# Kernel optimization log

Hardware: AMD Instinct MI355X
Metric: run time of the kernel (lower is better)

Reference implementation:

```python
import jax, jax.numpy as jnp
import numpy as np

N_NODES = 50000
N_EDGES = 800000
HIDDEN = 128
N_TYPES = 4
TIME_STEPS = [2]  # one layer, 2 propagation steps; residuals = {}


def setup_inputs() -> dict:
    key = jax.random.key(0)
    ks = jax.random.split(key, 8)
    std = HIDDEN ** (-0.5)
    states = jax.random.normal(ks[0], (N_NODES, HIDDEN), dtype=jnp.float32)
    etype = jax.random.randint(ks[1], (N_EDGES,), 0, N_TYPES, dtype=jnp.int32)
    src = jax.random.randint(ks[2], (N_EDGES,), 0, N_NODES, dtype=jnp.int32)
    tgt = jax.random.randint(ks[3], (N_EDGES,), 0, N_NODES, dtype=jnp.int32)
    edges = jnp.stack([etype, src, tgt], axis=1)  # [E, 3]: (type, source, target)
    type_weights = std * jax.random.normal(ks[4], (N_TYPES, HIDDEN, HIDDEN), dtype=jnp.float32)
    type_biases = std * jax.random.normal(ks[5], (N_TYPES, HIDDEN), dtype=jnp.float32)
    # Keras GRUCell (reset_after=True): kernel [H,3H], recurrent_kernel [H,3H], bias [2,3H]
    gru_kernel = std * jax.random.normal(ks[6], (HIDDEN, 3 * HIDDEN), dtype=jnp.float32)
    k7, k8 = jax.random.split(ks[7])
    gru_rec_kernel = std * jax.random.normal(k7, (HIDDEN, 3 * HIDDEN), dtype=jnp.float32)
    gru_bias = std * jax.random.normal(k8, (2, 3 * HIDDEN), dtype=jnp.float32)
    return {"states": states, "edges": edges, "type_weights": type_weights,
            "type_biases": type_biases, "gru_kernel": gru_kernel,
            "gru_rec_kernel": gru_rec_kernel, "gru_bias": gru_bias}


def _gru_cell(x, h, kernel, rec_kernel, bias):
    # Keras GRUCell with reset_after=True, tanh / sigmoid activations
    mx = x @ kernel + bias[0]          # [N, 3H]
    mh = h @ rec_kernel + bias[1]      # [N, 3H]
    xz, xr, xh = jnp.split(mx, 3, axis=-1)
    rz, rr, rh = jnp.split(mh, 3, axis=-1)
    z = jax.nn.sigmoid(xz + rz)
    r = jax.nn.sigmoid(xr + rr)
    hh = jnp.tanh(xh + r * rh)
    return z * h + (1.0 - z) * hh


def _propagate(h, etype, src, tgt, type_weights, type_biases, kernel, rec_kernel, bias):
    n_nodes = h.shape[0]
    xs = h[src]  # [E, H] gather of source states
    msg_e = jnp.zeros_like(xs)
    for t in range(N_TYPES):  # small fixed loop over edge types
        mask = (etype == t).astype(h.dtype)[:, None]
        msg_e = msg_e + mask * (xs @ type_weights[t] + type_biases[t])
    messages = jax.ops.segment_sum(msg_e, tgt, num_segments=n_nodes)  # scatter-add
    return _gru_cell(messages, h, kernel, rec_kernel, bias)


def reference(states, edges, type_weights, type_biases, gru_kernel, gru_rec_kernel, gru_bias):
    etype, src, tgt = edges[:, 0], edges[:, 1], edges[:, 2]
    h = states
    for steps in TIME_STEPS:  # single layer here (residuals empty)
        for _ in range(steps):
            h = _propagate(h, etype, src, tgt, type_weights, type_biases,
                           gru_kernel, gru_rec_kernel, gru_bias)
    return h
```

## Files before the change

### kernel.cpp

```cpp
#include <hip/hip_runtime.h>
#include <stdint.h>

namespace {
constexpr int kNodes = 50000;
constexpr int kEdges = 800000;
constexpr int kHid   = 128;
constexpr int kScanBlocks = (kNodes + 255) / 256;
constexpr int kBlocks64 = (kNodes + 63) / 64;

constexpr size_t oCounts    = 0;
constexpr size_t oCursor    = 200704;
constexpr size_t oBlockSums = 401408;
constexpr size_t oBpack     = 402432;
constexpr size_t oPacked    = 1057792;
constexpr size_t oMsg      = 4257792;
constexpr size_t oAux       = 17057792;
constexpr size_t oY         = 29857792;
constexpr size_t kWsNeeded   = oY + 51200000;
constexpr size_t kWsFallback = oY;

constexpr size_t bKhi = 0,      bKlo = 98304,  bRhi = 196608,
                 bRlo = 294912, bWhi = 393216, bWlo = 524288;
}

typedef __attribute__((ext_vector_type(8))) short short8;
typedef __attribute__((ext_vector_type(4))) float f32x4;

union ABFrag { short8 v; uint16_t u[8]; uint4 q; };

__device__ __forceinline__ uint16_t f2bf(float x) {
  uint32_t u = __float_as_uint(x);
  return (uint16_t)((u + 0x7FFFu + ((u >> 16) & 1u)) >> 16);
}
__device__ __forceinline__ float bf2f(uint16_t h) {
  return __uint_as_float(((uint32_t)h) << 16);
}

__device__ __forceinline__ float fast_rcp(float x) {
#if __has_builtin(__builtin_amdgcn_rcpf)
  return __builtin_amdgcn_rcpf(x);
#else
  return 1.f / x;
#endif
}
__device__ __forceinline__ float fast_exp2(float x) {
#if __has_builtin(__builtin_amdgcn_exp2f)
  return __builtin_amdgcn_exp2f(x);
#else
  return exp2f(x);
#endif
}
__device__ __forceinline__ float sigf(float x) {
  return fast_rcp(1.f + fast_exp2(-1.4426950408889634f * x));
}
__device__ __forceinline__ float tanh_fast(float x) {
  x = fminf(fmaxf(x, -10.f), 10.f);
  const float t = fast_exp2(2.8853900817779268f * x);
  return (t - 1.f) * fast_rcp(t + 1.f);
}

__device__ __forceinline__ int swz_pi(int p) {
  return (p & 64) | ((p & 3) << 4) | ((p >> 2) & 15);
}


__global__ __launch_bounds__(256) void count_kernel(const int* __restrict__ edges,
                                                    int* __restrict__ counts) {
  int e = blockIdx.x * 256 + threadIdx.x;
  if (e < kEdges) atomicAdd(&counts[edges[e * 3 + 2]], 1);
}

__global__ __launch_bounds__(256) void scan1_kernel(const int* __restrict__ counts,
                                                    int* __restrict__ cursor,
                                                    int* __restrict__ blocksums) {
  __shared__ int sd[256];
  const int t = threadIdx.x;
  const int i = blockIdx.x * 256 + t;
  int v = (i < kNodes) ? counts[i] : 0;
  sd[t] = v;
  __syncthreads();
  for (int off = 1; off < 256; off <<= 1) {
    int x = (t >= off) ? sd[t - off] : 0;
    __syncthreads();
    sd[t] += x;
    __syncthreads();
  }
  if (i < kNodes) cursor[i] = sd[t] - v;
  if (t == 255) blocksums[blockIdx.x] = sd[255];
}

__global__ __launch_bounds__(256) void scan2_kernel(int* __restrict__ blocksums,
                                                    int* __restrict__ boff,
                                                    int* __restrict__ bcur) {
  __shared__ int sd[256];
  const int t = threadIdx.x;
  int v = (t < kScanBlocks) ? blocksums[t] : 0;
  sd[t] = v;
  __syncthreads();
  for (int off = 1; off < 256; off <<= 1) {
    int x = (t >= off) ? sd[t - off] : 0;
    __syncthreads();
    sd[t] += x;
    __syncthreads();
  }
  if (t < kScanBlocks) {
    const int excl = sd[t] - v;
    blocksums[t] = excl;
    boff[t] = excl;
    bcur[t] = excl;
  }
  if (t == 0) boff[kScanBlocks] = kEdges;
}

__global__ __launch_bounds__(256) void scan3_kernel(int* __restrict__ cursor,
                                                    const int* __restrict__ blocksums) {
  const int i = blockIdx.x * 256 + threadIdx.x;
  if (i < kNodes) cursor[i] += blocksums[blockIdx.x];
}

__global__ __launch_bounds__(256) void bucket_scatter(
    const int* __restrict__ edges,
    int* __restrict__ bcur,
    unsigned long long* __restrict__ bkt) {
  __shared__ int hist[kScanBlocks];
  __shared__ int base[kScanBlocks];
  const int tid = threadIdx.x;
  const int e0 = blockIdx.x * 16000;
  const int e1 = min(e0 + 16000, kEdges);
  if (tid < kScanBlocks) hist[tid] = 0;
  __syncthreads();
  for (int e = e0 + tid; e < e1; e += 256)
    atomicAdd(&hist[edges[e * 3 + 2] >> 8], 1);
  __syncthreads();
  if (tid < kScanBlocks) {
    base[tid] = atomicAdd(&bcur[tid], hist[tid]);
    hist[tid] = 0;
  }
  __syncthreads();
  for (int e = e0 + tid; e < e1; e += 256) {
    const int et  = edges[e * 3 + 0];
    const int src = edges[e * 3 + 1];
    const int tgt = edges[e * 3 + 2];
    const int b = tgt >> 8;
    const int idx = atomicAdd(&hist[b], 1);
    bkt[base[b] + idx] =
        ((unsigned long long)(unsigned)tgt << 32) | (unsigned)(src * 4 + et);
  }
}

__global__ __launch_bounds__(256) void bucket_fill(
    const unsigned long long* __restrict__ bkt,
    const int* __restrict__ boff,
    const int* __restrict__ rowstart,
    unsigned* __restrict__ packed) {
  __shared__ int lcur[256];
  const int tid = threadIdx.x;
  const int b = blockIdx.x;
  const int nbase = b * 256;
  lcur[tid] = (nbase + tid < kNodes) ? rowstart[nbase + tid] : 0;
  __syncthreads();
  const int lo = boff[b], hi = boff[b + 1];
  for (int i = lo + tid; i < hi; i += 256) {
    const unsigned long long ent = bkt[i];
    const int tgt = (int)(ent >> 32);
    const int pos = atomicAdd(&lcur[tgt & 255], 1);
    packed[pos] = (unsigned)ent;
  }
}

__global__ __launch_bounds__(256) void fill_kernel(const int* __restrict__ edges,
                                                   int* __restrict__ cursor,
                                                   unsigned* __restrict__ packed) {
  int e = blockIdx.x * 256 + threadIdx.x;
  if (e < kEdges) {
    const int et  = edges[e * 3 + 0];
    const int src = edges[e * 3 + 1];
    const int tgt = edges[e * 3 + 2];
    const int pos = atomicAdd(&cursor[tgt], 1);
    packed[pos] = (unsigned)(src * 4 + et);
  }
}

__global__ __launch_bounds__(256) void pack_b_kernel(
    const float* __restrict__ K,
    const float* __restrict__ R,
    const float* __restrict__ W,
    uint16_t* __restrict__ bp) {
  const int idx = blockIdx.x * 256 + threadIdx.x;
  uint16_t* khi = bp + bKhi / 2;
  uint16_t* klo = bp + bKlo / 2;
  uint16_t* rhi = bp + bRhi / 2;
  uint16_t* rlo = bp + bRlo / 2;
  uint16_t* whi = bp + bWhi / 2;
  uint16_t* wlo = bp + bWlo / 2;
  if (idx < 128 * 384) {
    const int k = idx / 384, c = idx % 384;
    const int ksrc = swz_pi(k);
    const int kt = k >> 5, quad = (k >> 3) & 3, j = k & 7;
    const int nt = c >> 4, ln = (c & 15) | (quad << 4);
    const size_t o = ((size_t)(kt * 24 + nt) * 64 + ln) * 8 + j;
    const float kv = K[ksrc * 384 + c];
    const float rv = R[k * 384 + c];
    const uint16_t kh = f2bf(kv), rh = f2bf(rv);
    khi[o] = kh; klo[o] = f2bf(kv - bf2f(kh));
    rhi[o] = rh; rlo[o] = f2bf(rv - bf2f(rh));
  } else if (idx < 128 * 384 + 128 * 512) {
    const int i2 = idx - 128 * 384;
    const int k = i2 / 512, c = i2 % 512;
    const int t = c >> 7, cc = c & 127;
    const float wv = W[((size_t)t * 128 + k) * 128 + cc];
    const int kt = k >> 5, quad = (k >> 3) & 3, j = k & 7;
    const int nt = c >> 4, ln = (c & 15) | (quad << 4);
    const size_t o = ((size_t)(kt * 32 + nt) * 64 + ln) * 8 + j;
    const uint16_t wh = f2bf(wv);
    whi[o] = wh; wlo[o] = f2bf(wv - bf2f(wh));
  }
}

__device__ __forceinline__ void split8(const float* p, ABFrag& hi, ABFrag& lo) {
  const float4 a0 = *(const float4*)p;
  const float4 a1 = *(const float4*)(p + 4);
  const float v[8] = {a0.x, a0.y, a0.z, a0.w, a1.x, a1.y, a1.z, a1.w};
#pragma unroll
  for (int j = 0; j < 8; ++j) {
    const uint16_t t = f2bf(v[j]);
    hi.u[j] = t; lo.u[j] = f2bf(v[j] - bf2f(t));
  }
}
__device__ __forceinline__ void conv8(const float* p, ABFrag& hi) {
  const float4 a0 = *(const float4*)p;
  const float4 a1 = *(const float4*)(p + 4);
  const float v[8] = {a0.x, a0.y, a0.z, a0.w, a1.x, a1.y, a1.z, a1.w};
#pragma unroll
  for (int j = 0; j < 8; ++j) hi.u[j] = f2bf(v[j]);
}

__global__ __launch_bounds__(256, 3) void transform_mfma(
    const float* __restrict__ h,
    const uint16_t* __restrict__ bp,
    const float* __restrict__ TB,
    uint16_t* __restrict__ y16) {
  const int tid = threadIdx.x;
  const int w = tid >> 6;
  const int lane = tid & 63;
  const int col16 = lane & 15, quad = lane >> 4;
  const int b = blockIdx.x;
  const int half = (b >> 3) & 1;
  const int ng = (b & 7) | ((b >> 4) << 3);
  const int node0 = ng * 64;

  const uint4* __restrict__ Whi = (const uint4*)(bp + bWhi / 2);

  bool mok[4];
#pragma unroll
  for (int m = 0; m < 4; ++m) mok[m] = (node0 + m * 16) < kNodes;
  if (!mok[0]) return;

  f32x4 acc[4][4];
#pragma unroll
  for (int s = 0; s < 4; ++s)
#pragma unroll
    for (int m = 0; m < 4; ++m) acc[s][m] = (f32x4){0.f, 0.f, 0.f, 0.f};

  const float* hrow = h + (size_t)(node0 + col16) * kHid + quad * 8;

#pragma unroll
  for (int kt = 0; kt < 4; ++kt) {
    ABFrag ah[4], al[4];
#pragma unroll
    for (int m = 0; m < 4; ++m) {
      if (mok[m]) {
        split8(hrow + (size_t)m * 16 * kHid + kt * 32, ah[m], al[m]);
      } else {
        ah[m].q = make_uint4(0, 0, 0, 0); al[m].q = ah[m].q;
      }
    }
#pragma unroll
    for (int s = 0; s < 4; ++s) {
      ABFrag bh;
      bh.q = Whi[(size_t)(kt * 32 + w * 8 + half * 4 + s) * 64 + lane];
#pragma unroll
      for (int m = 0; m < 4; ++m) {
        f32x4 c = acc[s][m];
        c = __builtin_amdgcn_mfma_f32_16x16x32_bf16(ah[m].v, bh.v, c, 0, 0, 0);
        c = __builtin_amdgcn_mfma_f32_16x16x32_bf16(al[m].v, bh.v, c, 0, 0, 0);
        acc[s][m] = c;
      }
    }
  }

  float bias[4];
#pragma unroll
  for (int s = 0; s < 4; ++s) bias[s] = TB[w * 128 + (half * 4 + s) * 16 + col16];
#pragma unroll
  for (int m = 0; m < 4; ++m) {
    if (!mok[m]) continue;
#pragma unroll
    for (int r = 0; r < 4; ++r) {
      const int node = node0 + m * 16 + quad * 4 + r;
      const uint32_t lo = (uint32_t)f2bf(acc[0][m][r] + bias[0]) |
                          ((uint32_t)f2bf(acc[1][m][r] + bias[1]) << 16);
      const uint32_t hi = (uint32_t)f2bf(acc[2][m][r] + bias[2]) |
                          ((uint32_t)f2bf(acc[3][m][r] + bias[3]) << 16);
      const unsigned long long val = ((unsigned long long)hi << 32) | lo;
      __builtin_nontemporal_store(
          val, (unsigned long long*)&y16[(size_t)node * 512 + w * 128 +
                                         half * 64 + col16 * 4]);
    }
  }
}

__global__ __launch_bounds__(256) void gather_kernel(
    const uint32_t* __restrict__ y2,
    const uint32_t* __restrict__ packed,
    const int* __restrict__ rowstart,
    const int* __restrict__ counts,
    uint32_t* __restrict__ msg2) {
  const int tid = threadIdx.x;
  const int lane = tid & 63;
  const int v = blockIdx.x * 4 + (tid >> 6);
  const int cnt = counts[v];
  const int s0 = rowstart[v];
  float a0 = 0.f, a1 = 0.f;
  int e = 0;
  for (; e + 8 <= cnt; e += 8) {
    uint32_t p[8], u[8];
#pragma unroll
    for (int i = 0; i < 8; ++i) p[i] = packed[s0 + e + i];
#pragma unroll
    for (int i = 0; i < 8; ++i) u[i] = y2[(size_t)p[i] * 64 + lane];
#pragma unroll
    for (int i = 0; i < 8; ++i) {
      a0 += __uint_as_float(u[i] << 16);
      a1 += __uint_as_float(u[i] & 0xFFFF0000u);
    }
  }
  for (; e < cnt; ++e) {
    const uint32_t p = packed[s0 + e];
    const uint32_t u = y2[(size_t)p * 64 + lane];
    a0 += __uint_as_float(u << 16);
    a1 += __uint_as_float(u & 0xFFFF0000u);
  }
  msg2[(size_t)v * 64 + lane] = (uint32_t)f2bf(a0) | ((uint32_t)f2bf(a1) << 16);
}

__global__ __launch_bounds__(256, 2) void gru_mfma(
    const uint16_t* __restrict__ msg16,
    const float* __restrict__ hin,
    const uint16_t* __restrict__ bp,
    const float* __restrict__ gb,
    float* __restrict__ hout) {
  const int tid = threadIdx.x;
  const int w = tid >> 6;
  const int lane = tid & 63;
  const int col16 = lane & 15, quad = lane >> 4;
  const int node0 = blockIdx.x * 64;

  const uint4* __restrict__ Khi = (const uint4*)(bp + bKhi / 2);
  const uint4* __restrict__ Klo = (const uint4*)(bp + bKlo / 2);
  const uint4* __restrict__ Rhi = (const uint4*)(bp + bRhi / 2);
  const uint4* __restrict__ Rlo = (const uint4*)(bp + bRlo / 2);

  bool mok[4];
#pragma unroll
  for (int m = 0; m < 4; ++m) mok[m] = (node0 + m * 16) < kNodes;

  f32x4 aZ[2][4], aR[2][4], aX[2][4], aH[2][4];
#pragma unroll
  for (int i = 0; i < 2; ++i)
#pragma unroll
    for (int m = 0; m < 4; ++m) {
      aZ[i][m] = (f32x4){0.f, 0.f, 0.f, 0.f};
      aR[i][m] = aZ[i][m]; aX[i][m] = aZ[i][m]; aH[i][m] = aZ[i][m];
    }

  const uint16_t* mrow = msg16 + (size_t)(node0 + col16) * kHid + quad * 8;
  const float* hrow = hin + (size_t)(node0 + col16) * kHid + quad * 8;

#pragma unroll
  for (int kt = 0; kt < 4; ++kt) {
    ABFrag mh[4], hh[4];
#pragma unroll
    for (int m = 0; m < 4; ++m) {
      if (mok[m]) {
        mh[m].q = *(const uint4*)(mrow + (size_t)m * 16 * kHid + kt * 32);
        conv8(hrow + (size_t)m * 16 * kHid + kt * 32, hh[m]);
      } else {
        mh[m].q = make_uint4(0, 0, 0, 0); hh[m].q = mh[m].q;
      }
    }
#pragma unroll
    for (int lnt = 0; lnt < 2; ++lnt) {
      const int ntc = w * 2 + lnt;
      const size_t oz = (size_t)(kt * 24 + ntc) * 64 + lane;
      const size_t orr = (size_t)(kt * 24 + 8 + ntc) * 64 + lane;
      const size_t oh = (size_t)(kt * 24 + 16 + ntc) * 64 + lane;
      ABFrag kzh, kzl, rzh, rzl, krh, krl, rrh, rrl, khh, khl, rhh, rhl;
      kzh.q = Khi[oz]; kzl.q = Klo[oz]; rzh.q = Rhi[oz]; rzl.q = Rlo[oz];
      krh.q = Khi[orr]; krl.q = Klo[orr]; rrh.q = Rhi[orr]; rrl.q = Rlo[orr];
      khh.q = Khi[oh]; khl.q = Klo[oh]; rhh.q = Rhi[oh]; rhl.q = Rlo[oh];
#pragma unroll
      for (int m = 0; m < 4; ++m) {
        f32x4 z = aZ[lnt][m];
        z = __builtin_amdgcn_mfma_f32_16x16x32_bf16(mh[m].v, kzh.v, z, 0, 0, 0);
        z = __builtin_amdgcn_mfma_f32_16x16x32_bf16(mh[m].v, kzl.v, z, 0, 0, 0);
        z = __builtin_amdgcn_mfma_f32_16x16x32_bf16(hh[m].v, rzh.v, z, 0, 0, 0);
        z = __builtin_amdgcn_mfma_f32_16x16x32_bf16(hh[m].v, rzl.v, z, 0, 0, 0);
        aZ[lnt][m] = z;
        f32x4 r = aR[lnt][m];
        r = __builtin_amdgcn_mfma_f32_16x16x32_bf16(mh[m].v, krh.v, r, 0, 0, 0);
        r = __builtin_amdgcn_mfma_f32_16x16x32_bf16(mh[m].v, krl.v, r, 0, 0, 0);
        r = __builtin_amdgcn_mfma_f32_16x16x32_bf16(hh[m].v, rrh.v, r, 0, 0, 0);
        r = __builtin_amdgcn_mfma_f32_16x16x32_bf16(hh[m].v, rrl.v, r, 0, 0, 0);
        aR[lnt][m] = r;
        f32x4 x = aX[lnt][m];
        x = __builtin_amdgcn_mfma_f32_16x16x32_bf16(mh[m].v, khh.v, x, 0, 0, 0);
        x = __builtin_amdgcn_mfma_f32_16x16x32_bf16(mh[m].v, khl.v, x, 0, 0, 0);
        aX[lnt][m] = x;
        f32x4 y = aH[lnt][m];
        y = __builtin_amdgcn_mfma_f32_16x16x32_bf16(hh[m].v, rhh.v, y, 0, 0, 0);
        y = __builtin_amdgcn_mfma_f32_16x16x32_bf16(hh[m].v, rhl.v, y, 0, 0, 0);
        aH[lnt][m] = y;
      }
    }
  }

  __syncthreads();

#pragma unroll
  for (int lnt = 0; lnt < 2; ++lnt) {
    const int c = (w * 2 + lnt) * 16 + col16;
    const float bz = gb[c] + gb[384 + c];
    const float br = gb[128 + c] + gb[512 + c];
    const float bx = gb[256 + c];
    const float bh = gb[640 + c];
#pragma unroll
    for (int m = 0; m < 4; ++m) {
      if (!mok[m]) continue;
#pragma unroll
      for (int r = 0; r < 4; ++r) {
        const int node = node0 + m * 16 + quad * 4 + r;
        const float hp = hin[(size_t)node * kHid + c];
        const float z = sigf(aZ[lnt][m][r] + bz);
        const float rr = sigf(aR[lnt][m][r] + br);
        const float hh = tanh_fast(aX[lnt][m][r] + bx + rr * (aH[lnt][m][r] + bh));
        hout[(size_t)node * kHid + c] = z * hp + (1.f - z) * hh;
      }
    }
  }
}


__global__ __launch_bounds__(256, 2) void message_fb_kernel(
    const float* __restrict__ hin,
    const unsigned* __restrict__ packed,
    const int* __restrict__ rowend,
    const int* __restrict__ counts,
    const float* __restrict__ W,
    const float* __restrict__ TB,
    float* __restrict__ msg) {
  __shared__ float S[32 * 512];
  __shared__ int D[32][4];
  const int tid = threadIdx.x;
  {
    const int g = tid >> 7;
    const int j = tid & 127;
    for (int i = 0; i < 16; ++i) {
      const int nl = g * 16 + i;
      const int v = blockIdx.x * 32 + nl;
      if (v >= kNodes) break;
      const int cnt = counts[v];
      const int s0 = rowend[v] - cnt;
      float a0 = 0.f, a1 = 0.f, a2 = 0.f, a3 = 0.f;
      int d0 = 0, d1 = 0, d2 = 0, d3 = 0;
      for (int e = 0; e < cnt; ++e) {
        const unsigned p = packed[s0 + e];
        const int src = (int)(p >> 2);
        const int t = (int)(p & 3u);
        const float val = hin[(size_t)src * kHid + j];
        a0 += (t == 0) ? val : 0.f;
        a1 += (t == 1) ? val : 0.f;
        a2 += (t == 2) ? val : 0.f;
        a3 += (t == 3) ? val : 0.f;
        d0 += (t == 0); d1 += (t == 1); d2 += (t == 2); d3 += (t == 3);
      }
      float* Sn = &S[nl * 512];
      Sn[j] = a0; Sn[128 + j] = a1; Sn[256 + j] = a2; Sn[384 + j] = a3;
      if (j == 0) { D[nl][0] = d0; D[nl][1] = d1; D[nl][2] = d2; D[nl][3] = d3; }
    }
  }
  __syncthreads();

  const int lane = tid & 31;
  const int jj = lane * 4;
  const int n0 = (tid >> 5) * 4;
  float acc[4][4] = {};
  const float4* __restrict__ W4 = (const float4*)W;
  for (int tk = 0; tk < 512; tk += 4) {
    const float4 w0 = W4[(size_t)(tk + 0) * 32 + lane];
    const float4 w1 = W4[(size_t)(tk + 1) * 32 + lane];
    const float4 w2 = W4[(size_t)(tk + 2) * 32 + lane];
    const float4 w3 = W4[(size_t)(tk + 3) * 32 + lane];
#pragma unroll
    for (int n = 0; n < 4; ++n) {
      const float4 s = *(const float4*)&S[(n0 + n) * 512 + tk];
      acc[n][0] += s.x * w0.x + s.y * w1.x + s.z * w2.x + s.w * w3.x;
      acc[n][1] += s.x * w0.y + s.y * w1.y + s.z * w2.y + s.w * w3.y;
      acc[n][2] += s.x * w0.z + s.y * w1.z + s.z * w2.z + s.w * w3.z;
      acc[n][3] += s.x * w0.w + s.y * w1.w + s.z * w2.w + s.w * w3.w;
    }
  }
  const float4 B0 = *(const float4*)&TB[0 * 128 + jj];
  const float4 B1 = *(const float4*)&TB[1 * 128 + jj];
  const float4 B2 = *(const float4*)&TB[2 * 128 + jj];
  const float4 B3 = *(const float4*)&TB[3 * 128 + jj];
#pragma unroll
  for (int n = 0; n < 4; ++n) {
    const int v = blockIdx.x * 32 + n0 + n;
    if (v < kNodes) {
      float4 o;
      const float d0 = (float)D[n0 + n][0], d1 = (float)D[n0 + n][1];
      const float d2 = (float)D[n0 + n][2], d3 = (float)D[n0 + n][3];
      o.x = acc[n][0] + d0 * B0.x + d1 * B1.x + d2 * B2.x + d3 * B3.x;
      o.y = acc[n][1] + d0 * B0.y + d1 * B1.y + d2 * B2.y + d3 * B3.y;
      o.z = acc[n][2] + d0 * B0.z + d1 * B1.z + d2 * B2.z + d3 * B3.z;
      o.w = acc[n][3] + d0 * B0.w + d1 * B1.w + d2 * B2.w + d3 * B3.w;
      *(float4*)&msg[(size_t)v * kHid + jj] = o;
    }
  }
}

__global__ __launch_bounds__(256, 2) void gru_fb_kernel(
    const float* __restrict__ msg,
    const float* __restrict__ hin,
    const float* __restrict__ K,
    const float* __restrict__ R,
    const float* __restrict__ gb,
    float* __restrict__ hout) {
  __shared__ float At[2][16][68];
  __shared__ float Bt[2][16][384];
  const int tid = threadIdx.x;
  const int node0 = blockIdx.x * 64;
  const int cg = tid >> 4;
  const int ng = tid & 15;

  float accZ[4][8] = {}, accR[4][8] = {}, accXH[4][8] = {}, accRH[4][8] = {};
  const float4* __restrict__ K4 = (const float4*)K;
  const float4* __restrict__ R4 = (const float4*)R;
  const int sn = tid >> 2;
  const int sj = tid & 3;

  for (int k0 = 0; k0 < 128; k0 += 16) {
    __syncthreads();
    {
      float4 vm = make_float4(0.f, 0.f, 0.f, 0.f);
      float4 vh = vm;
      const int node = node0 + sn;
      if (node < kNodes) {
        vm = *(const float4*)&msg[(size_t)node * kHid + k0 + sj * 4];
        vh = *(const float4*)&hin[(size_t)node * kHid + k0 + sj * 4];
      }
      At[0][sj * 4 + 0][sn] = vm.x; At[0][sj * 4 + 1][sn] = vm.y;
      At[0][sj * 4 + 2][sn] = vm.z; At[0][sj * 4 + 3][sn] = vm.w;
      At[1][sj * 4 + 0][sn] = vh.x; At[1][sj * 4 + 1][sn] = vh.y;
      At[1][sj * 4 + 2][sn] = vh.z; At[1][sj * 4 + 3][sn] = vh.w;
    }
#pragma unroll
    for (int i = 0; i < 6; ++i) {
      const int idx = tid + i * 256;
      const int row = idx / 96;
      const int c4 = idx - row * 96;
      *(float4*)&Bt[0][row][c4 * 4] = K4[(size_t)(k0 + row) * 96 + c4];
      *(float4*)&Bt[1][row][c4 * 4] = R4[(size_t)(k0 + row) * 96 + c4];
    }
    __syncthreads();

    for (int kk = 0; kk < 16; ++kk) {
      const float4 am4 = *(const float4*)&At[0][kk][ng * 4];
      const float4 ah4 = *(const float4*)&At[1][kk][ng * 4];
      const float am[4] = {am4.x, am4.y, am4.z, am4.w};
      const float ah[4] = {ah4.x, ah4.y, ah4.z, ah4.w};
      const int cb = cg * 8;
#pragma unroll
      for (int gset = 0; gset < 3; ++gset) {
        const int off = gset * 128 + cb;
        const float4 k0v = *(const float4*)&Bt[0][kk][off];
        const float4 k1v = *(const float4*)&Bt[0][kk][off + 4];
        const float4 r0v = *(const float4*)&Bt[1][kk][off];
        const float4 r1v = *(const float4*)&Bt[1][kk][off + 4];
        const float bk[8] = {k0v.x, k0v.y, k0v.z, k0v.w, k1v.x, k1v.y, k1v.z, k1v.w};
        const float br[8] = {r0v.x, r0v.y, r0v.z, r0v.w, r1v.x, r1v.y, r1v.z, r1v.w};
        if (gset == 0) {
#pragma unroll
          for (int n = 0; n < 4; ++n)
#pragma unroll
            for (int c = 0; c < 8; ++c) accZ[n][c] += am[n] * bk[c] + ah[n] * br[c];
        } else if (gset == 1) {
#pragma unroll
          for (int n = 0; n < 4; ++n)
#pragma unroll
            for (int c = 0; c < 8; ++c) accR[n][c] += am[n] * bk[c] + ah[n] * br[c];
        } else {
#pragma unroll
          for (int n = 0; n < 4; ++n)
#pragma unroll
            for (int c = 0; c < 8; ++c) {
              accXH[n][c] += am[n] * bk[c];
              accRH[n][c] += ah[n] * br[c];
            }
        }
      }
    }
  }

  const int cb = cg * 8;
#pragma unroll
  for (int n = 0; n < 4; ++n) {
    const int node = node0 + ng * 4 + n;
    if (node >= kNodes) continue;
    float o[8];
#pragma unroll
    for (int c = 0; c < 8; ++c) {
      const float z = sigf(accZ[n][c] + gb[cb + c] + gb[384 + cb + c]);
      const float r = sigf(accR[n][c] + gb[128 + cb + c] + gb[512 + cb + c]);
      const float hh = tanh_fast(accXH[n][c] + gb[256 + cb + c] +
                                 r * (accRH[n][c] + gb[640 + cb + c]));
      const float hp = hin[(size_t)node * kHid + cb + c];
      o[c] = z * hp + (1.f - z) * hh;
    }
    *(float4*)&hout[(size_t)node * kHid + cb]     = make_float4(o[0], o[1], o[2], o[3]);
    *(float4*)&hout[(size_t)node * kHid + cb + 4] = make_float4(o[4], o[5], o[6], o[7]);
  }
}

extern "C" void kernel_launch(void* const* d_in, const int* in_sizes, int n_in,
                              void* d_out, int out_size, void* d_ws, size_t ws_size,
                              hipStream_t stream) {
  const float* states = (const float*)d_in[0];
  const int*   edges  = (const int*)d_in[1];
  const float* W      = (const float*)d_in[2];
  const float* TB     = (const float*)d_in[3];
  const float* K      = (const float*)d_in[4];
  const float* R      = (const float*)d_in[5];
  const float* gb     = (const float*)d_in[6];
  float* out = (float*)d_out;

  if (ws_size < kWsFallback) return;

  char* ws = (char*)d_ws;
  int*      counts  = (int*)(ws + oCounts);
  int*      cursor  = (int*)(ws + oCursor);
  int*      bsums   = (int*)(ws + oBlockSums);
  uint16_t* bpack   = (uint16_t*)(ws + oBpack);
  unsigned* packed  = (unsigned*)(ws + oPacked);
  float*    msgf    = (float*)(ws + oMsg);
  uint16_t* msg16   = (uint16_t*)(ws + oMsg);
  uint32_t* msg2    = (uint32_t*)(ws + oMsg);
  int*      boff    = (int*)(ws + oAux);
  int*      bcur    = (int*)(ws + oAux + 1024);
  uint16_t* y16     = (uint16_t*)(ws + oY);
  uint32_t* y2      = (uint32_t*)(ws + oY);
  unsigned long long* bkt = (unsigned long long*)(ws + oY);

  hipMemsetAsync(counts, 0, 200704, stream);
  count_kernel<<<kEdges / 256, 256, 0, stream>>>(edges, counts);
  scan1_kernel<<<kScanBlocks, 256, 0, stream>>>(counts, cursor, bsums);
  scan2_kernel<<<1, 256, 0, stream>>>(bsums, boff, bcur);
  scan3_kernel<<<kScanBlocks, 256, 0, stream>>>(cursor, bsums);

  if (ws_size >= kWsNeeded) {
    bucket_scatter<<<50, 256, 0, stream>>>(edges, bcur, bkt);
    bucket_fill<<<kScanBlocks, 256, 0, stream>>>(bkt, boff, cursor, packed);
    pack_b_kernel<<<448, 256, 0, stream>>>(K, R, W, bpack);
    const int tf_blocks = 1568;
    const int ga_blocks = kNodes / 4;
    transform_mfma<<<tf_blocks, 256, 0, stream>>>(states, bpack, TB, y16);
    gather_kernel<<<ga_blocks, 256, 0, stream>>>(y2, packed, cursor, counts, msg2);
    gru_mfma<<<kBlocks64, 256, 0, stream>>>(msg16, states, bpack, gb, out);
    transform_mfma<<<tf_blocks, 256, 0, stream>>>(out, bpack, TB, y16);
    gather_kernel<<<ga_blocks, 256, 0, stream>>>(y2, packed, cursor, counts, msg2);
    gru_mfma<<<kBlocks64, 256, 0, stream>>>(msg16, out, bpack, gb, out);
  } else {
    fill_kernel<<<(kEdges + 255) / 256, 256, 0, stream>>>(edges, cursor, packed);
    const int msg_blocks = (kNodes + 31) / 32;
    const int gru_blocks = (kNodes + 63) / 64;
    message_fb_kernel<<<msg_blocks, 256, 0, stream>>>(states, packed, cursor,
                                                      counts, W, TB, msgf);
    gru_fb_kernel<<<gru_blocks, 256, 0, stream>>>(msgf, states, K, R, gb, out);
    message_fb_kernel<<<msg_blocks, 256, 0, stream>>>(out, packed, cursor,
                                                      counts, W, TB, msgf);
    gru_fb_kernel<<<gru_blocks, 256, 0, stream>>>(msgf, out, K, R, gb, out);
  }
}
```

Measured before the change: 437.8 us.

## Fuse neighbor gather into GRU kernel via shared-memory message tile

Moves the per-node bf16 message gather-sum into the start of the GRU MFMA kernel, storing the 64-node message tile in LDS instead of writing and rereading a global message buffer. This removes one launch per step and a round trip of the message array through global memory. Each wave now gathers 16 nodes sequentially over a much smaller grid, which reduces parallelism available to hide random gather latency.

```diff
diff --git a/kernel.cpp b/kernel.cpp
--- a/kernel.cpp
+++ b/kernel.cpp
@@ -310,52 +310,53 @@
   }
 }
 
-__global__ __launch_bounds__(256) void gather_kernel(
+__global__ __launch_bounds__(256, 2) void gru_mfma(
     const uint32_t* __restrict__ y2,
     const uint32_t* __restrict__ packed,
     const int* __restrict__ rowstart,
     const int* __restrict__ counts,
-    uint32_t* __restrict__ msg2) {
-  const int tid = threadIdx.x;
-  const int lane = tid & 63;
-  const int v = blockIdx.x * 4 + (tid >> 6);
-  const int cnt = counts[v];
-  const int s0 = rowstart[v];
-  float a0 = 0.f, a1 = 0.f;
-  int e = 0;
-  for (; e + 8 <= cnt; e += 8) {
-    uint32_t p[8], u[8];
-#pragma unroll
-    for (int i = 0; i < 8; ++i) p[i] = packed[s0 + e + i];
-#pragma unroll
-    for (int i = 0; i < 8; ++i) u[i] = y2[(size_t)p[i] * 64 + lane];
-#pragma unroll
-    for (int i = 0; i < 8; ++i) {
-      a0 += __uint_as_float(u[i] << 16);
-      a1 += __uint_as_float(u[i] & 0xFFFF0000u);
-    }
-  }
-  for (; e < cnt; ++e) {
-    const uint32_t p = packed[s0 + e];
-    const uint32_t u = y2[(size_t)p * 64 + lane];
-    a0 += __uint_as_float(u << 16);
-    a1 += __uint_as_float(u & 0xFFFF0000u);
-  }
-  msg2[(size_t)v * 64 + lane] = (uint32_t)f2bf(a0) | ((uint32_t)f2bf(a1) << 16);
-}
-
-__global__ __launch_bounds__(256, 2) void gru_mfma(
-    const uint16_t* __restrict__ msg16,
     const float* __restrict__ hin,
     const uint16_t* __restrict__ bp,
     const float* __restrict__ gb,
     float* __restrict__ hout) {
+  __shared__ uint32_t Lm[64 * 72];
   const int tid = threadIdx.x;
   const int w = tid >> 6;
   const int lane = tid & 63;
   const int col16 = lane & 15, quad = lane >> 4;
   const int node0 = blockIdx.x * 64;
 
+  for (int i = 0; i < 16; ++i) {
+    const int ln = w * 16 + i;
+    const int v = node0 + ln;
+    if (v < kNodes) {
+      const int cnt = counts[v];
+      const int s0 = rowstart[v];
+      float a0 = 0.f, a1 = 0.f;
+      int e = 0;
+      for (; e + 8 <= cnt; e += 8) {
+        uint32_t p[8], u[8];
+#pragma unroll
+        for (int k = 0; k < 8; ++k) p[k] = packed[s0 + e + k];
+#pragma unroll
+        for (int k = 0; k < 8; ++k) u[k] = y2[(size_t)p[k] * 64 + lane];
+#pragma unroll
+        for (int k = 0; k < 8; ++k) {
+          a0 += __uint_as_float(u[k] << 16);
+          a1 += __uint_as_float(u[k] & 0xFFFF0000u);
+        }
+      }
+      for (; e < cnt; ++e) {
+        const uint32_t p = packed[s0 + e];
+        const uint32_t u = y2[(size_t)p * 64 + lane];
+        a0 += __uint_as_float(u << 16);
+        a1 += __uint_as_float(u & 0xFFFF0000u);
+      }
+      Lm[ln * 72 + lane] = (uint32_t)f2bf(a0) | ((uint32_t)f2bf(a1) << 16);
+    }
+  }
+  __syncthreads();
+
   const uint4* __restrict__ Khi = (const uint4*)(bp + bKhi / 2);
   const uint4* __restrict__ Klo = (const uint4*)(bp + bKlo / 2);
   const uint4* __restrict__ Rhi = (const uint4*)(bp + bRhi / 2);
@@ -374,7 +375,6 @@
       aR[i][m] = aZ[i][m]; aX[i][m] = aZ[i][m]; aH[i][m] = aZ[i][m];
     }
 
-  const uint16_t* mrow = msg16 + (size_t)(node0 + col16) * kHid + quad * 8;
   const float* hrow = hin + (size_t)(node0 + col16) * kHid + quad * 8;
 
 #pragma unroll
@@ -383,7 +383,7 @@
 #pragma unroll
     for (int m = 0; m < 4; ++m) {
       if (mok[m]) {
-        mh[m].q = *(const uint4*)(mrow + (size_t)m * 16 * kHid + kt * 32);
+        mh[m].q = *(const uint4*)&Lm[(m * 16 + col16) * 72 + quad * 4 + kt * 16];
         conv8(hrow + (size_t)m * 16 * kHid + kt * 32, hh[m]);
       } else {
         mh[m].q = make_uint4(0, 0, 0, 0); hh[m].q = mh[m].q;
@@ -654,8 +654,6 @@
   uint16_t* bpack   = (uint16_t*)(ws + oBpack);
   unsigned* packed  = (unsigned*)(ws + oPacked);
   float*    msgf    = (float*)(ws + oMsg);
-  uint16_t* msg16   = (uint16_t*)(ws + oMsg);
-  uint32_t* msg2    = (uint32_t*)(ws + oMsg);
   int*      boff    = (int*)(ws + oAux);
   int*      bcur    = (int*)(ws + oAux + 1024);
   uint16_t* y16     = (uint16_t*)(ws + oY);
@@ -673,13 +671,12 @@
     bucket_fill<<<kScanBlocks, 256, 0, stream>>>(bkt, boff, cursor, packed);
     pack_b_kernel<<<448, 256, 0, stream>>>(K, R, W, bpack);
     const int tf_blocks = 1568;
-    const int ga_blocks = kNodes / 4;
     transform_mfma<<<tf_blocks, 256, 0, stream>>>(states, bpack, TB, y16);
-    gather_kernel<<<ga_blocks, 256, 0, stream>>>(y2, packed, cursor, counts, msg2);
-    gru_mfma<<<kBlocks64, 256, 0, stream>>>(msg16, states, bpack, gb, out);
+    gru_mfma<<<kBlocks64, 256, 0, stream>>>(y2, packed, cursor, counts,
+                                            states, bpack, gb, out);
     transform_mfma<<<tf_blocks, 256, 0, stream>>>(out, bpack, TB, y16);
-    gather_kernel<<<ga_blocks, 256, 0, stream>>>(y2, packed, cursor, counts, msg2);
-    gru_mfma<<<kBlocks64, 256, 0, stream>>>(msg16, out, bpack, gb, out);
+    gru_mfma<<<kBlocks64, 256, 0, stream>>>(y2, packed, cursor, counts,
+                                            out, bpack, gb, out);
   } else {
     fill_kernel<<<(kEdges + 255) / 256, 256, 0, stream>>>(edges, cursor, packed);
     const int msg_blocks = (kNodes + 31) / 32;
```

New measurement: 579.1 us. 32.3% more time.
